# Performance work log

Measured on AMD Instinct MI355X. Metric: run time of the kernel, lower is better.

Reference implementation:

```python
import jax, jax.numpy as jnp
import numpy as np

# Module hyperparameters (init_kwargs): shape_data = [n_t, n_y, n_x]
N_T, N_Y, N_X = 5, 32, 32
N = N_Y * N_X            # nb_nodes
DX = DY = DT = 1.0


def setup_inputs() -> dict:
    key = jax.random.key(0)
    k1, k2, k3 = jax.random.split(key, 3)
    n_b = 4
    kappa = jax.random.uniform(k1, (n_b, 1, N, N_T), dtype=jnp.float32)
    m = jax.random.normal(k2, (n_b, 2, N, N_T), dtype=jnp.float32)
    H = jax.random.normal(k3, (n_b, 2, 2, N, N_T), dtype=jnp.float32)
    return {"kappa": kappa, "m": m, "H": H}


def _stencil_indices():
    # 9-point stencil on the n_y x n_x grid; row-major node index = y*n_x + x.
    yy, xx = np.meshgrid(np.arange(N_Y), np.arange(N_X), indexing="ij")
    yy, xx = yy.reshape(-1), xx.reshape(-1)
    node = np.arange(N)
    offs = [(0, 0), (0, 1), (0, -1), (1, 0), (-1, 0), (1, 1), (1, -1), (-1, 1), (-1, -1)]
    rows, cols, valid = [], [], []
    for oy, ox in offs:
        ny, nx = yy + oy, xx + ox
        ok = (ny >= 0) & (ny < N_Y) & (nx >= 0) & (nx < N_X)
        rows.append(node)
        cols.append(np.where(ok, ny * N_X + nx, node))
        valid.append(ok.astype(np.float32))
    return (jnp.asarray(np.concatenate(rows)),
            jnp.asarray(np.concatenate(cols)),
            jnp.asarray(np.concatenate(valid)))

ROWS, COLS, VALID = _stencil_indices()


def _build_A(kappa, m, H):
    # Finite-difference discretization of A = kappa^2 I + m.grad - div(H grad)
    # kappa: [b,t,N]; m: [b,t,2,N]; H: [b,t,2,2,N]
    mx, my = m[..., 0, :], m[..., 1, :]
    H11, H22 = H[..., 0, 0, :], H[..., 1, 1, :]
    H12 = 0.5 * (H[..., 0, 1, :] + H[..., 1, 0, :])
    c0 = kappa ** 2 + 2.0 * H11 / DX ** 2 + 2.0 * H22 / DY ** 2   # center
    cpx = mx / (2 * DX) - H11 / DX ** 2                           # (0,+1)
    cmx = -mx / (2 * DX) - H11 / DX ** 2                          # (0,-1)
    cpy = my / (2 * DY) - H22 / DY ** 2                           # (+1,0)
    cmy = -my / (2 * DY) - H22 / DY ** 2                          # (-1,0)
    cc = H12 / (2 * DX * DY)                                      # cross term
    # order matches _stencil_indices offsets
    vals = jnp.concatenate([c0, cpx, cmx, cpy, cmy, -cc, cc, cc, -cc], axis=-1)
    vals = vals * VALID                                           # zero out-of-grid neighbors
    b, t = vals.shape[0], vals.shape[1]
    A = jnp.zeros((b, t, N, N), vals.dtype)
    return A.at[:, :, ROWS, COLS].add(vals)


def reference(kappa, m, H):
    # rearrange to [batch, time, ...] leading
    kap = jnp.transpose(kappa[:, 0], (0, 2, 1))          # [b,t,N]
    mm = jnp.transpose(m, (0, 3, 1, 2))                  # [b,t,2,N]
    HH = jnp.transpose(H, (0, 4, 1, 2, 3))               # [b,t,2,2,N]
    A = _build_A(kap, mm, HH)                            # [b,t,N,N]
    I = jnp.eye(N, dtype=A.dtype)
    M = I + DT * A                                       # M_k = Id + dt * A_k
    MM = jnp.einsum("btij,btjk->btik", M, M)             # spspmm(M_k, M_k)
    b = M.shape[0]
    Q = jnp.zeros((b, N_T * N, N_T * N), A.dtype)
    # block-tridiagonal precision matrix assembly (QR = Id)
    Q = Q.at[:, 0:N, 0:N].set(MM[:, 0])
    Q = Q.at[:, 0:N, N:2 * N].set(-M[:, 1])
    for i in range(1, N_T - 1):
        Q = Q.at[:, i * N:(i + 1) * N, (i - 1) * N:i * N].set(-M[:, i - 1])
        Q = Q.at[:, i * N:(i + 1) * N, i * N:(i + 1) * N].set(MM[:, i] + I)
        Q = Q.at[:, i * N:(i + 1) * N, (i + 1) * N:(i + 2) * N].set(-M[:, i + 1])
    i = N_T - 1
    Q = Q.at[:, i * N:(i + 1) * N, (i - 1) * N:i * N].set(-M[:, i - 1])
    Q = Q.at[:, i * N:(i + 1) * N, i * N:(i + 1) * N].set(MM[:, i])
    return Q
```

## Files before the change

### kernel.cpp

```cpp
#include <hip/hip_runtime.h>

#define NT   5
#define NY   32
#define NX   32
#define NN   1024
#define QDIM 5120
#define NB   4

__device__ __forceinline__ void stencil9(const float* __restrict__ kap,
                                         const float* __restrict__ m,
                                         const float* __restrict__ H,
                                         int b, int t, int n, float s[9]) {
    float k   = kap[((size_t)b * NN + n) * NT + t];
    float mx  = m[(((size_t)b * 2 + 0) * NN + n) * NT + t];
    float my  = m[(((size_t)b * 2 + 1) * NN + n) * NT + t];
    float H11 = H[((((size_t)b * 2 + 0) * 2 + 0) * NN + n) * NT + t];
    float H01 = H[((((size_t)b * 2 + 0) * 2 + 1) * NN + n) * NT + t];
    float H10 = H[((((size_t)b * 2 + 1) * 2 + 0) * NN + n) * NT + t];
    float H22 = H[((((size_t)b * 2 + 1) * 2 + 1) * NN + n) * NT + t];
    float cc = 0.25f * (H01 + H10);
    s[0] = 1.0f + k * k + 2.0f * H11 + 2.0f * H22;
    s[1] =  0.5f * mx - H11;
    s[2] = -0.5f * mx - H11;
    s[3] =  0.5f * my - H22;
    s[4] = -0.5f * my - H22;
    s[5] = -cc;
    s[6] =  cc;
    s[7] =  cc;
    s[8] = -cc;
    int y = n >> 5, x = n & 31;
    if (x == NX - 1) { s[1] = 0.f; s[5] = 0.f; s[7] = 0.f; }
    if (x == 0)      { s[2] = 0.f; s[6] = 0.f; s[8] = 0.f; }
    if (y == NY - 1) { s[3] = 0.f; s[5] = 0.f; s[6] = 0.f; }
    if (y == 0)      { s[4] = 0.f; s[7] = 0.f; s[8] = 0.f; }
}

__global__ __launch_bounds__(256) void spde_scatter(const float* __restrict__ kap,
                                                    const float* __restrict__ m,
                                                    const float* __restrict__ H,
                                                    float* __restrict__ Q) {
    int tid = blockIdx.x * blockDim.x + threadIdx.x;
    if (tid >= NB * NT * NN) return;
    int r  = tid & (NN - 1);
    int bt = tid >> 10;
    int t  = bt % NT;
    int b  = bt / NT;

    const int oy[9] = {0, 0, 0, 1, -1, 1, 1, -1, -1};
    const int ox[9] = {0, 1, -1, 0, 0, 1, -1, 1, -1};

    float sr[9];
    stencil9(kap, m, H, b, t, r, sr);
    int ry = r >> 5, rx = r & 31;

    float acc[5][5];
#pragma unroll
    for (int i = 0; i < 5; ++i)
#pragma unroll
        for (int j = 0; j < 5; ++j) acc[i][j] = 0.f;

#pragma unroll
    for (int d1 = 0; d1 < 9; ++d1) {
        float a = sr[d1];
        int ky = ry + oy[d1], kx = rx + ox[d1];
        bool valid = ((unsigned)ky < NY) && ((unsigned)kx < NX);
        int k = valid ? (ky * NX + kx) : r;
        float sk[9];
        stencil9(kap, m, H, b, t, k, sk);
#pragma unroll
        for (int d2 = 0; d2 < 9; ++d2) {
            acc[oy[d1] + oy[d2] + 2][ox[d1] + ox[d2] + 2] += a * sk[d2];
        }
    }
    if (t >= 1 && t <= NT - 2) acc[2][2] += 1.0f;

    size_t brow = (size_t)b * QDIM * QDIM;

    {
        size_t rowoff = brow + (size_t)(t * NN + r) * QDIM + (size_t)t * NN;
#pragma unroll
        for (int dy = -2; dy <= 2; ++dy) {
            int cy = ry + dy;
            if ((unsigned)cy >= NY) continue;
#pragma unroll
            for (int dx = -2; dx <= 2; ++dx) {
                int cx = rx + dx;
                if ((unsigned)cx >= NX) continue;
                Q[rowoff + cy * NX + cx] = acc[dy + 2][dx + 2];
            }
        }
    }

#pragma unroll
    for (int d = 0; d < 9; ++d) {
        int cy = ry + oy[d], cx = rx + ox[d];
        if ((unsigned)cy >= NY || (unsigned)cx >= NX) continue;
        int c = cy * NX + cx;
        float v = -sr[d];
        if (t >= 1)
            Q[brow + (size_t)((t - 1) * NN + r) * QDIM + (size_t)t * NN + c] = v;
        if (t <= NT - 2)
            Q[brow + (size_t)((t + 1) * NN + r) * QDIM + (size_t)t * NN + c] = v;
    }
}

extern "C" void kernel_launch(void* const* d_in, const int* in_sizes, int n_in,
                              void* d_out, int out_size, void* d_ws, size_t ws_size,
                              hipStream_t stream) {
    const float* kap = (const float*)d_in[0];
    const float* m   = (const float*)d_in[1];
    const float* H   = (const float*)d_in[2];
    float* Q = (float*)d_out;

    hipMemsetAsync(d_out, 0, (size_t)out_size * sizeof(float), stream);

    int total = NB * NT * NN;
    spde_scatter<<<(total + 255) / 256, 256, 0, stream>>>(kap, m, H, Q);
}
```

Baseline: 436.4 us.

## Fuse zero-fill into a row-per-block kernel writing full Q rows with float4

Drops the separate memset of the dense output and launches one block per output row. Each block computes its stencil products in shared memory, then writes the entire 5120-wide row, zeros and non-zeros alike, with coalesced float4 stores. This removes the second pass over the roughly 420 MB output and the scattered non-coalesced writes. In exchange it launches 20480 small blocks, each paying a few synchronisations and redundant per-row stencil recomputation done by only a handful of threads.

```diff
diff --git a/kernel.cpp b/kernel.cpp
--- a/kernel.cpp
+++ b/kernel.cpp
@@ -6,6 +6,9 @@
 #define NN   1024
 #define QDIM 5120
 #define NB   4
+
+__device__ const int c_oy[9] = {0, 0, 0, 1, -1, 1, 1, -1, -1};
+__device__ const int c_ox[9] = {0, 1, -1, 0, 0, 1, -1, 1, -1};
 
 __device__ __forceinline__ void stencil9(const float* __restrict__ kap,
                                          const float* __restrict__ m,
@@ -35,72 +38,93 @@
     if (y == 0)      { s[4] = 0.f; s[7] = 0.f; s[8] = 0.f; }
 }
 
-__global__ __launch_bounds__(256) void spde_scatter(const float* __restrict__ kap,
-                                                    const float* __restrict__ m,
-                                                    const float* __restrict__ H,
-                                                    float* __restrict__ Q) {
-    int tid = blockIdx.x * blockDim.x + threadIdx.x;
-    if (tid >= NB * NT * NN) return;
-    int r  = tid & (NN - 1);
-    int bt = tid >> 10;
-    int t  = bt % NT;
-    int b  = bt / NT;
-
+__global__ __launch_bounds__(256) void spde_fused(const float* __restrict__ kap,
+                                                  const float* __restrict__ m,
+                                                  const float* __restrict__ H,
+                                                  float* __restrict__ Q) {
     const int oy[9] = {0, 0, 0, 1, -1, 1, 1, -1, -1};
     const int ox[9] = {0, 1, -1, 0, 0, 1, -1, 1, -1};
 
-    float sr[9];
-    stencil9(kap, m, H, b, t, r, sr);
+    int row = blockIdx.x;
+    int b = row / (NT * NN);
+    int g = row - b * (NT * NN);
+    int t = g >> 10;
+    int r = g & (NN - 1);
     int ry = r >> 5, rx = r & 31;
+    int tid = threadIdx.x;
 
-    float acc[5][5];
-#pragma unroll
-    for (int i = 0; i < 5; ++i)
-#pragma unroll
-        for (int j = 0; j < 5; ++j) acc[i][j] = 0.f;
+    __shared__ float sk[9][9];
+    __shared__ float moff[2][9];
+    __shared__ float accL[25];
 
-#pragma unroll
-    for (int d1 = 0; d1 < 9; ++d1) {
-        float a = sr[d1];
-        int ky = ry + oy[d1], kx = rx + ox[d1];
+    if (tid < 9) {
+        int ky = ry + c_oy[tid], kx = rx + c_ox[tid];
         bool valid = ((unsigned)ky < NY) && ((unsigned)kx < NX);
         int k = valid ? (ky * NX + kx) : r;
-        float sk[9];
-        stencil9(kap, m, H, b, t, k, sk);
+        float s[9];
+        stencil9(kap, m, H, b, t, k, s);
 #pragma unroll
-        for (int d2 = 0; d2 < 9; ++d2) {
-            acc[oy[d1] + oy[d2] + 2][ox[d1] + ox[d2] + 2] += a * sk[d2];
-        }
+        for (int e = 0; e < 9; ++e)
+            sk[tid][(oy[e] + 1) * 3 + (ox[e] + 1)] = s[e];
+    } else if (tid == 9) {
+        float s[9] = {0,0,0,0,0,0,0,0,0};
+        if (t >= 1) stencil9(kap, m, H, b, t - 1, r, s);
+#pragma unroll
+        for (int e = 0; e < 9; ++e)
+            moff[0][(oy[e] + 1) * 3 + (ox[e] + 1)] = -s[e];
+    } else if (tid == 10) {
+        float s[9] = {0,0,0,0,0,0,0,0,0};
+        if (t <= NT - 2) stencil9(kap, m, H, b, t + 1, r, s);
+#pragma unroll
+        for (int e = 0; e < 9; ++e)
+            moff[1][(oy[e] + 1) * 3 + (ox[e] + 1)] = -s[e];
     }
-    if (t >= 1 && t <= NT - 2) acc[2][2] += 1.0f;
+    __syncthreads();
 
-    size_t brow = (size_t)b * QDIM * QDIM;
-
-    {
-        size_t rowoff = brow + (size_t)(t * NN + r) * QDIM + (size_t)t * NN;
+    if (tid < 25) {
+        int dy = tid / 5 - 2, dx = tid % 5 - 2;
+        float a = 0.f;
 #pragma unroll
-        for (int dy = -2; dy <= 2; ++dy) {
-            int cy = ry + dy;
-            if ((unsigned)cy >= NY) continue;
-#pragma unroll
-            for (int dx = -2; dx <= 2; ++dx) {
-                int cx = rx + dx;
-                if ((unsigned)cx >= NX) continue;
-                Q[rowoff + cy * NX + cx] = acc[dy + 2][dx + 2];
+        for (int d1 = 0; d1 < 9; ++d1) {
+            int dy2 = dy - oy[d1], dx2 = dx - ox[d1];
+            if (dy2 >= -1 && dy2 <= 1 && dx2 >= -1 && dx2 <= 1) {
+                a += sk[0][(oy[d1] + 1) * 3 + (ox[d1] + 1)]
+                   * sk[d1][(dy2 + 1) * 3 + (dx2 + 1)];
             }
         }
+        if (tid == 12 && t >= 1 && t <= NT - 2) a += 1.0f;
+        accL[tid] = a;
     }
+    __syncthreads();
 
+    size_t base = ((size_t)b * QDIM + g) * QDIM;
 #pragma unroll
-    for (int d = 0; d < 9; ++d) {
-        int cy = ry + oy[d], cx = rx + ox[d];
-        if ((unsigned)cy >= NY || (unsigned)cx >= NX) continue;
-        int c = cy * NX + cx;
-        float v = -sr[d];
-        if (t >= 1)
-            Q[brow + (size_t)((t - 1) * NN + r) * QDIM + (size_t)t * NN + c] = v;
-        if (t <= NT - 2)
-            Q[brow + (size_t)((t + 1) * NN + r) * QDIM + (size_t)t * NN + c] = v;
+    for (int kk = 0; kk < 5; ++kk) {
+        int slot = tid + kk * 256;
+        int c0 = slot * 4;
+        int j  = c0 >> 10;
+        int o  = c0 & (NN - 1);
+        int dy = (o >> 5) - ry;
+        int dx0 = (o & 31) - rx;
+        float4 v = make_float4(0.f, 0.f, 0.f, 0.f);
+        float* ve = &v.x;
+        if (j == t) {
+            if (dy >= -2 && dy <= 2) {
+#pragma unroll
+                for (int e = 0; e < 4; ++e) {
+                    int dx = dx0 + e;
+                    if (dx >= -2 && dx <= 2) ve[e] = accL[(dy + 2) * 5 + (dx + 2)];
+                }
+            }
+        } else if ((j == t - 1 || j == t + 1) && dy >= -1 && dy <= 1) {
+            int z = (j > t) ? 1 : 0;
+#pragma unroll
+            for (int e = 0; e < 4; ++e) {
+                int dx = dx0 + e;
+                if (dx >= -1 && dx <= 1) ve[e] = moff[z][(dy + 1) * 3 + (dx + 1)];
+            }
+        }
+        *(float4*)(Q + base + c0) = v;
     }
 }
 
@@ -112,8 +136,6 @@
     const float* H   = (const float*)d_in[2];
     float* Q = (float*)d_out;
 
-    hipMemsetAsync(d_out, 0, (size_t)out_size * sizeof(float), stream);
-
-    int total = NB * NT * NN;
-    spde_scatter<<<(total + 255) / 256, 256, 0, stream>>>(kap, m, H, Q);
+    int nrows = NB * NT * NN;
+    spde_fused<<<nrows, 256, 0, stream>>>(kap, m, H, Q);
 }
```

Result: faster. 417.6 us (-4.3%).
